# Kernel tuning notes

Measured on AMD Instinct MI355X. Metric: run time of the kernel, lower is better.

## Reference

```python
import jax, jax.numpy as jnp
import numpy as np
from jax import lax

H, HD, P, C, HID = 8, 64, 16, 512, 2048
ALIBI_ALPHA, START_I = 1.0, 0
EPS = 1e-5

def setup_inputs():
    key = jax.random.key(0)
    ks = jax.random.split(key, 20)
    s = 0.02
    return {
        "x": jax.random.normal(ks[0], (8, 1024, C), jnp.float32),
        "Wq": jax.random.normal(ks[1], (HD, HD), jnp.float32) * s,
        "Wk": jax.random.normal(ks[2], (HD, HD), jnp.float32) * s,
        "Wv": jax.random.normal(ks[3], (HD, HD), jnp.float32) * s,
        "Wo": jax.random.normal(ks[4], (C, C), jnp.float32) * s,
        "bo": jnp.zeros((C,), jnp.float32),
        "th_pre": jax.random.normal(ks[5], (H, H), jnp.float32) * (1.0 / np.sqrt(H)),
        "th_post": jax.random.normal(ks[6], (H, H), jnp.float32) * (1.0 / np.sqrt(H)),
        "p_keys": jax.random.normal(ks[7], (P, 1, HD), jnp.float32) * s,
        "p_values": jax.random.normal(ks[8], (P, 1, HD), jnp.float32) * s,
        "conv1_w": jax.random.normal(ks[9], (2 * HID, C, 3), jnp.float32) * s,
        "conv1_b": jnp.zeros((2 * HID,), jnp.float32),
        "conv2_w": jax.random.normal(ks[10], (C, HID, 3), jnp.float32) * s,
        "conv2_b": jnp.zeros((C,), jnp.float32),
        "ln1_g": jnp.ones((C,), jnp.float32),
        "ln1_b": jnp.zeros((C,), jnp.float32),
        "ln2_g": jnp.ones((C,), jnp.float32),
        "ln2_b": jnp.zeros((C,), jnp.float32),
    }

def _layernorm(x, g, b):
    mu = jnp.mean(x, axis=-1, keepdims=True)
    var = jnp.mean((x - mu) ** 2, axis=-1, keepdims=True)
    return (x - mu) * lax.rsqrt(var + EPS) * g + b

def _mha(x, Wq, Wk, Wv, Wo, bo, th_pre, th_post, p_keys, p_values):
    N, L, _ = x.shape
    xh = x.reshape(N, L, H, HD)
    q = xh @ Wq.T  # per-head-dim linear, as in torch (applied to last dim)
    k = xh @ Wk.T
    v = xh @ Wv.T
    # persistent memory: [P,1,HD] broadcast over batch and heads
    pk = jnp.broadcast_to(p_keys[None], (N, P, H, HD))
    pv = jnp.broadcast_to(p_values[None], (N, P, H, HD))
    k = jnp.concatenate([k, pk], axis=1)  # (N, L+P, H, HD)
    v = jnp.concatenate([v, pv], axis=1)
    energy = jnp.einsum('nqhd,nkhd->nhqk', q, k)
    # ALiBi: slope_h = 2^(-alpha*(h+1+start_i)), bias = -|q-k|*slope, zero on persistent cols
    slopes = 2.0 ** (-ALIBI_ALPHA * (jnp.arange(1, H + 1, dtype=jnp.float32) + START_I))
    t = jnp.arange(L, dtype=jnp.float32)
    dist = jnp.abs(t[:, None] - t[None, :])  # (L, L)
    bias = -dist[None, :, :] * slopes[:, None, None]  # (H, L, L)
    bias = jnp.pad(bias, ((0, 0), (0, 0), (0, P)))
    energy = energy + bias[None]
    energy = jnp.einsum('gh,nhqk->ngqk', th_pre, energy)  # pre-softmax talking heads (1x1 conv)
    attn = jax.nn.softmax(energy / jnp.sqrt(jnp.float32(C)), axis=-1)
    attn = jnp.einsum('gh,nhqk->ngqk', th_post, attn)  # post-softmax talking heads
    out = jnp.einsum('nhql,nlhd->nqhd', attn, v).reshape(N, L, C)
    return out @ Wo.T + bo

def _ffn(x, conv1_w, conv1_b, conv2_w, conv2_b):
    dn = ('NCH', 'OIH', 'NCH')
    xc = jnp.transpose(x, (0, 2, 1))  # (N, C, L)
    xp = jnp.pad(xc, ((0, 0), (0, 0), (1, 1)))  # same padding, k=3
    h = lax.conv_general_dilated(xp, conv1_w, (1,), 'VALID', dimension_numbers=dn) + conv1_b[None, :, None]
    h1, h2 = jnp.split(h, 2, axis=1)
    h = jax.nn.silu(h1) * h2  # swiglu
    hp = jnp.pad(h, ((0, 0), (0, 0), (1, 1)))
    y = lax.conv_general_dilated(hp, conv2_w, (1,), 'VALID', dimension_numbers=dn) + conv2_b[None, :, None]
    return jnp.transpose(y, (0, 2, 1))

def reference(x, Wq, Wk, Wv, Wo, bo, th_pre, th_post, p_keys, p_values,
              conv1_w, conv1_b, conv2_w, conv2_b, ln1_g, ln1_b, ln2_g, ln2_b):
    a = _mha(x, Wq, Wk, Wv, Wo, bo, th_pre, th_post, p_keys, p_values)
    x1 = _layernorm(a + x, ln1_g, ln1_b)
    f = _ffn(x1, conv1_w, conv1_b, conv2_w, conv2_b)
    return _layernorm(f + x1, ln2_g, ln2_b)
```

## Files before the change

kernel.cpp:

```cpp
#include <hip/hip_runtime.h>
#include <cstddef>
#include <cstdint>

#define NB   8
#define LQ   1024
#define CH   512
#define HHE  8
#define HDD  64
#define PPM  16
#define LP   1040
#define HID  2048

typedef unsigned short ushort_t;
typedef __attribute__((ext_vector_type(8))) short short8;
typedef __attribute__((ext_vector_type(4))) float floatx4;

static const size_t O_QB   = 0;
static const size_t O_KB   = 2097152;
static const size_t O_VB   = 4227072;
static const size_t O_VT   = 6356992;
static const size_t O_AOB  = 8486912;
static const size_t O_AF   = 10584064;
static const size_t O_X1B  = 16777216;
static const size_t O_HPAD = 18878464;
static const size_t O_W1   = 27283456;
static const size_t O_W2   = 30429184;
static const size_t O_WO   = 32002048;

__device__ __forceinline__ ushort_t f2bf(float f) {
  uint32_t u = __float_as_uint(f);
  u += 0x7FFFu + ((u >> 16) & 1u);
  return (ushort_t)(u >> 16);
}
__device__ __forceinline__ float bf2f(ushort_t h) {
  return __uint_as_float(((uint32_t)h) << 16);
}

__device__ __forceinline__ void async16(ushort_t* lds, const ushort_t* g) {
  __builtin_amdgcn_global_load_lds(
      (const __attribute__((address_space(1))) void*)g,
      (__attribute__((address_space(3))) void*)lds, 16, 0, 0);
}

__global__ __launch_bounds__(256) void pack_bf16_kernel(
    const float* __restrict__ src, ushort_t* __restrict__ dst,
    int K, int KD, int icShift)
{
  const int oc = blockIdx.x;
  const int icMask = (1 << icShift) - 1;
  for (int k = threadIdx.x; k < K; k += 256) {
    int ic = k & icMask, dl = k >> icShift;
    dst[(size_t)oc * K + k] = f2bf(src[(size_t)oc * K + ic * KD + dl]);
  }
}

template<int EPI>
__global__ __launch_bounds__(256, 2) void mfma_gemm(
    const ushort_t* __restrict__ Ab, const ushort_t* __restrict__ Bb,
    int K, int BS, int P, int NOUT,
    const float* __restrict__ bias, const float* __restrict__ res,
    float* __restrict__ outf, ushort_t* __restrict__ outh)
{
  __shared__ ushort_t As[128 * 32];
  __shared__ ushort_t Bs[128 * 32];
  const int t = threadIdx.x;
  const int w = t >> 6, l = t & 63;
  const int m0 = blockIdx.x * 128, n0 = blockIdx.y * 128;

  const int kChunk = K / (int)gridDim.z;
  const int kstart = blockIdx.z * kChunk;

  const int sub = l >> 2;
  const int kc8 = (l & 3) * 8;
  const ushort_t* aptr[2];
  const ushort_t* bptr[2];
  #pragma unroll
  for (int c = 0; c < 2; ++c) {
    int arow = m0 + w * 32 + c * 16 + sub;
    aptr[c] = Ab + (size_t)(arow >> 10) * BS + (size_t)(arow & 1023) * P + kc8 + kstart;
    int brow = n0 + w * 32 + c * 16 + sub;
    bptr[c] = Bb + (size_t)brow * K + kc8 + kstart;
  }

  const int wm = w >> 1, wn = w & 1;
  const int lm = l & 15, q = l >> 4;
  floatx4 acc[4][4];
  #pragma unroll
  for (int i = 0; i < 4; ++i)
    #pragma unroll
    for (int j = 0; j < 4; ++j)
      acc[i][j] = (floatx4){0.f, 0.f, 0.f, 0.f};

  const int kIters = kChunk >> 5;
  for (int kt = 0; kt < kIters; ++kt) {
    __syncthreads();
    async16(&As[w * 1024 +   0], aptr[0]);
    async16(&As[w * 1024 + 512], aptr[1]);
    async16(&Bs[w * 1024 +   0], bptr[0]);
    async16(&Bs[w * 1024 + 512], bptr[1]);
    aptr[0] += 32; aptr[1] += 32; bptr[0] += 32; bptr[1] += 32;
    __syncthreads();
    short8 af[4], bf[4];
    #pragma unroll
    for (int i = 0; i < 4; ++i)
      af[i] = *(const short8*)&As[(wm * 64 + i * 16 + lm) * 32 + q * 8];
    #pragma unroll
    for (int i = 0; i < 4; ++i)
      bf[i] = *(const short8*)&Bs[(wn * 64 + i * 16 + lm) * 32 + q * 8];
    #pragma unroll
    for (int i = 0; i < 4; ++i)
      #pragma unroll
      for (int j = 0; j < 4; ++j)
        acc[i][j] = __builtin_amdgcn_mfma_f32_16x16x32_bf16(af[i], bf[j], acc[i][j], 0, 0, 0);
  }

  #pragma unroll
  for (int i = 0; i < 4; ++i) {
    #pragma unroll
    for (int j = 0; j < 4; ++j) {
      const int mbase = m0 + wm * 64 + i * 16 + q * 4;
      const int n = n0 + wn * 64 + j * 16 + lm;
      #pragma unroll
      for (int r = 0; r < 4; ++r) {
        const int m = mbase + r;
        float v = acc[i][j][r];
        if (EPI == 0) {
          outh[(size_t)m * NOUT + n] = f2bf(v);
        } else if (EPI == 1) {
          outf[(size_t)m * NOUT + n] = v + bias[n];
        } else if (EPI == 2) {
          outf[(size_t)m * NOUT + n] = v + bias[n] + res[(size_t)m * NOUT + n];
        } else {
          outf[(size_t)blockIdx.z * 4194304 + (size_t)m * NOUT + n] = v;
        }
      }
    }
  }
}

__global__ __launch_bounds__(256) void ksum_kernel(
    float* __restrict__ pb, const float* __restrict__ bias)
{
  const size_t i = ((size_t)blockIdx.x * 256 + threadIdx.x) * 4;
  float4 a = *(const float4*)&pb[i];
  float4 b = *(const float4*)&pb[i +  4194304];
  float4 c = *(const float4*)&pb[i +  8388608];
  float4 d = *(const float4*)&pb[i + 12582912];
  const int col = (int)(i & 511);
  float4 bi = *(const float4*)&bias[col];
  float4 o;
  o.x = a.x + b.x + c.x + d.x + bi.x;
  o.y = a.y + b.y + c.y + d.y + bi.y;
  o.z = a.z + b.z + c.z + d.z + bi.z;
  o.w = a.w + b.w + c.w + d.w + bi.w;
  *(float4*)&pb[i] = o;
}

__global__ __launch_bounds__(256) void qkv_mfma(
    const float* __restrict__ x,
    const float* __restrict__ Wq, const float* __restrict__ Wk, const float* __restrict__ Wv,
    ushort_t* __restrict__ qo, ushort_t* __restrict__ ko, ushort_t* __restrict__ vo)
{
  __shared__ ushort_t Ws[8 * 512];
  const int mat = blockIdx.y;
  const float* __restrict__ W = (mat == 0) ? Wq : (mat == 1) ? Wk : Wv;
  const int t = threadIdx.x;

  for (int e = t; e < 4096; e += 256) {
    const int oc = e >> 6, ic = e & 63;
    const int nt = oc >> 4, lmm = oc & 15, s = ic >> 5, qd = (ic >> 3) & 3, j = ic & 7;
    Ws[(((nt * 2 + s) * 4 + qd) * 16 + lmm) * 8 + j] = f2bf(W[e]);
  }

  const int w = t >> 6, l = t & 63;
  const int lm = l & 15, quad = l >> 4;
  const int tok0 = blockIdx.x * 64 + w * 16;

  short8 af[16];
  {
    const float* xrow = x + (size_t)(tok0 + lm) * CH + quad * 8;
    #pragma unroll
    for (int h = 0; h < 8; ++h) {
      #pragma unroll
      for (int s = 0; s < 2; ++s) {
        const float4 a = *(const float4*)(xrow + h * 64 + s * 32);
        const float4 b = *(const float4*)(xrow + h * 64 + s * 32 + 4);
        short8 f;
        f[0] = (short)f2bf(a.x); f[1] = (short)f2bf(a.y);
        f[2] = (short)f2bf(a.z); f[3] = (short)f2bf(a.w);
        f[4] = (short)f2bf(b.x); f[5] = (short)f2bf(b.y);
        f[6] = (short)f2bf(b.z); f[7] = (short)f2bf(b.w);
        af[h * 2 + s] = f;
      }
    }
  }
  __syncthreads();

  short8 bfr[8];
  #pragma unroll
  for (int nt = 0; nt < 4; ++nt)
    #pragma unroll
    for (int s = 0; s < 2; ++s)
      bfr[nt * 2 + s] = *(const short8*)&Ws[((nt * 2 + s) * 64 + l) * 8];

  const int n = tok0 >> 10, lpos = tok0 & 1023;
  ushort_t* outp;
  size_t base;
  if (mat == 0) { base = ((size_t)n * LQ + lpos) * CH; outp = qo; }
  else          { base = ((size_t)n * LP + lpos) * CH; outp = (mat == 1) ? ko : vo; }

  #pragma unroll
  for (int h = 0; h < 8; ++h) {
    floatx4 acc[4];
    #pragma unroll
    for (int nt = 0; nt < 4; ++nt) acc[nt] = (floatx4){0.f, 0.f, 0.f, 0.f};
    #pragma unroll
    for (int nt = 0; nt < 4; ++nt)
      #pragma unroll
      for (int s = 0; s < 2; ++s)
        acc[nt] = __builtin_amdgcn_mfma_f32_16x16x32_bf16(
            af[h * 2 + s], bfr[nt * 2 + s], acc[nt], 0, 0, 0);
    #pragma unroll
    for (int nt = 0; nt < 4; ++nt)
      #pragma unroll
      for (int r = 0; r < 4; ++r)
        outp[base + (size_t)(quad * 4 + r) * CH + h * 64 + nt * 16 + lm] =
            f2bf(acc[nt][r]);
  }
}

__global__ __launch_bounds__(256) void persist_kernel(
    const float* __restrict__ pk, const float* __restrict__ pv,
    ushort_t* __restrict__ ko, ushort_t* __restrict__ vo)
{
  const int t = blockIdx.x * 256 + threadIdx.x;
  const int n = t >> 13, p = (t >> 9) & 15, c = t & 511, d = c & 63;
  const size_t o = ((size_t)n * LP + LQ + p) * CH + c;
  ko[o] = f2bf(pk[p * 64 + d]);
  vo[o] = f2bf(pv[p * 64 + d]);
}

__global__ __launch_bounds__(256) void vtrans_kernel(
    const ushort_t* __restrict__ Vb, ushort_t* __restrict__ VT)
{
  __shared__ ushort_t Ls[16 * 520];
  const int n = blockIdx.y, k0 = blockIdx.x * 16;
  const int t = threadIdx.x;
  const int r = t >> 4;
  {
    const ushort_t* src = Vb + ((size_t)(n * LP + k0 + r)) * 512 + (t & 15) * 8;
    ushort_t* dst = &Ls[r * 520 + (t & 15) * 8];
    #pragma unroll
    for (int it = 0; it < 4; ++it)
      *(short8*)(dst + it * 128) = *(const short8*)(src + it * 128);
  }
  __syncthreads();
  #pragma unroll
  for (int rep = 0; rep < 2; ++rep) {
    const int d = t + rep * 256;
    short8 v0, v1;
    #pragma unroll
    for (int j = 0; j < 8; ++j) {
      v0[j] = (short)Ls[j * 520 + d];
      v1[j] = (short)Ls[(8 + j) * 520 + d];
    }
    ushort_t* dst = VT + ((size_t)(n * 512 + d)) * LP + k0;
    *(short8*)(dst)     = v0;
    *(short8*)(dst + 8) = v1;
  }
}

__global__ __launch_bounds__(256, 2) void attn_mfma(
    const ushort_t* __restrict__ Qb, const ushort_t* __restrict__ Kb,
    const ushort_t* __restrict__ VT,
    const float* __restrict__ thpre, const float* __restrict__ thpost,
    ushort_t* __restrict__ aob)
{
  __shared__ __align__(16) char smem[38912];
  float* Ps  = (float*)smem;
  float* Eb0 = (float*)(smem + 18432);
  float* Eb1 = (float*)(smem + 28672);
  float* Ohn = (float*)smem;

  const int n = blockIdx.y, q0 = blockIdx.x * 16;
  const int t = threadIdx.x;
  const int w = t >> 6, l = t & 63;
  const int lm = l & 15, quad = l >> 4;
  const float invs = 0.044194173824159216f;

  short8 qf[4];
  {
    const ushort_t* qrow = Qb + ((size_t)(n * LQ + q0 + lm)) * 512 + (w * 2) * 64 + quad * 8;
    qf[0] = *(const short8*)(qrow);
    qf[1] = *(const short8*)(qrow + 32);
    qf[2] = *(const short8*)(qrow + 64);
    qf[3] = *(const short8*)(qrow + 96);
  }

  float tps[2][8], psl[2], tpo[2][8];
  #pragma unroll
  for (int gg = 0; gg < 2; ++gg) {
    const int g = w * 2 + gg;
    float ps = 0.f;
    #pragma unroll
    for (int h = 0; h < 8; ++h) {
      float tv = thpre[g * 8 + h] * invs;
      tps[gg][h] = tv;
      ps += tv * (1.0f / (float)(2 << h));
      tpo[gg][h] = thpost[g * 8 + h];
    }
    psl[gg] = ps;
  }

  float m_[2][4], z_[2][4];
  #pragma unroll
  for (int gg = 0; gg < 2; ++gg)
    #pragma unroll
    for (int r = 0; r < 4; ++r) { m_[gg][r] = -1e30f; z_[gg][r] = 0.f; }

  floatx4 o_[2][4];
  #pragma unroll
  for (int gg = 0; gg < 2; ++gg)
    #pragma unroll
    for (int ch = 0; ch < 4; ++ch) o_[gg][ch] = (floatx4){0.f, 0.f, 0.f, 0.f};

  const ushort_t* kg = Kb + ((size_t)(n * LP + lm)) * 512 + (w * 2) * 64 + quad * 8;
  const ushort_t* vg0 = VT + ((size_t)(n * 512) + (w * 2 + 0) * 64 + lm) * LP;
  const ushort_t* vg1 = VT + ((size_t)(n * 512) + (w * 2 + 1) * 64 + lm) * LP;

  short8 kfE[4], kfO[4], vpf[8];

  auto loadKg = [&](short8 (&r)[4], int step) {
    const ushort_t* p = kg + (size_t)step * 8192;
    r[0] = *(const short8*)(p);
    r[1] = *(const short8*)(p + 32);
    r[2] = *(const short8*)(p + 64);
    r[3] = *(const short8*)(p + 96);
  };
  auto loadV = [&](int p) {
    int ko = 32 * p + quad * 8;
    if (ko > 1032) ko = 1032;
    #pragma unroll
    for (int ch = 0; ch < 4; ++ch) {
      vpf[ch]     = *(const short8*)(vg0 + (size_t)(ch * 16) * LP + ko);
      vpf[4 + ch] = *(const short8*)(vg1 + (size_t)(ch * 16) * LP + ko);
    }
  };

  auto qktE = [&](short8 (&kf)[4], float* Eb) {
    #pragma unroll
    for (int hh = 0; hh < 2; ++hh) {
      floatx4 e = (floatx4){0.f, 0.f, 0.f, 0.f};
      e = __builtin_amdgcn_mfma_f32_16x16x32_bf16(qf[hh * 2 + 0], kf[hh * 2 + 0], e, 0, 0, 0);
      e = __builtin_amdgcn_mfma_f32_16x16x32_bf16(qf[hh * 2 + 1], kf[hh * 2 + 1], e, 0, 0, 0);
      *(floatx4*)&Eb[(((w * 2 + hh) * 16 + lm)) * 20 + quad * 4] = e;
    }
  };

  auto online2 = [&](int p) {
    float s0[2][4], s1[2][4];
    #pragma unroll
    for (int gg = 0; gg < 2; ++gg)
      #pragma unroll
      for (int r = 0; r < 4; ++r) { s0[gg][r] = 0.f; s1[gg][r] = 0.f; }
    #pragma unroll
    for (int h = 0; h < 8; ++h) {
      const floatx4 a = *(const floatx4*)&Eb0[(h * 16 + lm) * 20 + quad * 4];
      const floatx4 b = *(const floatx4*)&Eb1[(h * 16 + lm) * 20 + quad * 4];
      #pragma unroll
      for (int gg = 0; gg < 2; ++gg) {
        const float tv = tps[gg][h];
        #pragma unroll
        for (int r = 0; r < 4; ++r) {
          s0[gg][r] += tv * a[r];
          s1[gg][r] += tv * b[r];
        }
      }
    }
    const int k0 = 32 * p;
    float pm[2][4];
    #pragma unroll
    for (int r = 0; r < 4; ++r) {
      const float qpos = (float)(q0 + quad * 4 + r);
      const float d0 = fabsf(qpos - (float)(k0 + lm));
      const float d1 = fabsf(qpos - (float)(k0 + 16 + lm));
      #pragma unroll
      for (int gg = 0; gg < 2; ++gg) {
        s0[gg][r] -= d0 * psl[gg];
        s1[gg][r] -= d1 * psl[gg];
        pm[gg][r] = fmaxf(s0[gg][r], s1[gg][r]);
      }
    }
    #pragma unroll
    for (int off = 1; off < 16; off <<= 1)
      #pragma unroll
      for (int gg = 0; gg < 2; ++gg)
        #pragma unroll
        for (int r = 0; r < 4; ++r)
          pm[gg][r] = fmaxf(pm[gg][r], __shfl_xor(pm[gg][r], off));
    float sc[2][4];
    #pragma unroll
    for (int gg = 0; gg < 2; ++gg)
      #pragma unroll
      for (int r = 0; r < 4; ++r) {
        const float mn = fmaxf(m_[gg][r], pm[gg][r]);
        sc[gg][r] = __expf(m_[gg][r] - mn);
        const float p0 = __expf(s0[gg][r] - mn);
        const float p1 = __expf(s1[gg][r] - mn);
        z_[gg][r] = z_[gg][r] * sc[gg][r] + p0 + p1;
        m_[gg][r] = mn;
        float* prow = &Ps[((w * 2 + gg) * 16 + quad * 4 + r) * 36];
        prow[lm] = p0;
        prow[16 + lm] = p1;
      }
    #pragma unroll
    for (int gg = 0; gg < 2; ++gg)
      #pragma unroll
      for (int ch = 0; ch < 4; ++ch)
        #pragma unroll
        for (int r = 0; r < 4; ++r)
          o_[gg][ch][r] *= sc[gg][r];
  };

  auto online1 = [&]() {
    float s0[2][4];
    #pragma unroll
    for (int gg = 0; gg < 2; ++gg)
      #pragma unroll
      for (int r = 0; r < 4; ++r) s0[gg][r] = 0.f;
    #pragma unroll
    for (int h = 0; h < 8; ++h) {
      const floatx4 a = *(const floatx4*)&Eb0[(h * 16 + lm) * 20 + quad * 4];
      #pragma unroll
      for (int gg = 0; gg < 2; ++gg) {
        const float tv = tps[gg][h];
        #pragma unroll
        for (int r = 0; r < 4; ++r) s0[gg][r] += tv * a[r];
      }
    }
    float pm[2][4];
    #pragma unroll
    for (int gg = 0; gg < 2; ++gg)
      #pragma unroll
      for (int r = 0; r < 4; ++r) pm[gg][r] = s0[gg][r];
    #pragma unroll
    for (int off = 1; off < 16; off <<= 1)
      #pragma unroll
      for (int gg = 0; gg < 2; ++gg)
        #pragma unroll
        for (int r = 0; r < 4; ++r)
          pm[gg][r] = fmaxf(pm[gg][r], __shfl_xor(pm[gg][r], off));
    float sc[2][4];
    #pragma unroll
    for (int gg = 0; gg < 2; ++gg)
      #pragma unroll
      for (int r = 0; r < 4; ++r) {
        const float mn = fmaxf(m_[gg][r], pm[gg][r]);
        sc[gg][r] = __expf(m_[gg][r] - mn);
        const float p0 = __expf(s0[gg][r] - mn);
        z_[gg][r] = z_[gg][r] * sc[gg][r] + p0;
        m_[gg][r] = mn;
        float* prow = &Ps[((w * 2 + gg) * 16 + quad * 4 + r) * 36];
        prow[lm] = p0;
        prow[16 + lm] = 0.f;
      }
    #pragma unroll
    for (int gg = 0; gg < 2; ++gg)
      #pragma unroll
      for (int ch = 0; ch < 4; ++ch)
        #pragma unroll
        for (int r = 0; r < 4; ++r)
          o_[gg][ch][r] *= sc[gg][r];
  };

  auto pv = [&]() {
    #pragma unroll
    for (int gg = 0; gg < 2; ++gg) {
      const float4 pa = *(const float4*)&Ps[((w * 2 + gg) * 16 + lm) * 36 + quad * 8];
      const float4 pb = *(const float4*)&Ps[((w * 2 + gg) * 16 + lm) * 36 + quad * 8 + 4];
      short8 pk;
      pk[0] = (short)f2bf(pa.x); pk[1] = (short)f2bf(pa.y);
      pk[2] = (short)f2bf(pa.z); pk[3] = (short)f2bf(pa.w);
      pk[4] = (short)f2bf(pb.x); pk[5] = (short)f2bf(pb.y);
      pk[6] = (short)f2bf(pb.z); pk[7] = (short)f2bf(pb.w);
      #pragma unroll
      for (int ch = 0; ch < 4; ++ch)
        o_[gg][ch] = __builtin_amdgcn_mfma_f32_16x16x32_bf16(
            pk, vpf[gg * 4 + ch], o_[gg][ch], 0, 0, 0);
    }
  };

  loadKg(kfE, 0);
  loadKg(kfO, 1);
  loadV(0);

  for (int p = 0; p < 32; ++p) {
    qktE(kfE, Eb0);
    qktE(kfO, Eb1);
    loadKg(kfE, 2 * p + 2);
    if (p < 31) loadKg(kfO, 2 * p + 3);
    __syncthreads();
    online2(p);
    __syncthreads();
    pv();
    loadV(p + 1);
  }
  qktE(kfE, Eb0);
  __syncthreads();
  online1();
  __syncthreads();
  pv();

  #pragma unroll
  for (int off = 1; off < 16; off <<= 1)
    #pragma unroll
    for (int gg = 0; gg < 2; ++gg)
      #pragma unroll
      for (int r = 0; r < 4; ++r)
        z_[gg][r] += __shfl_xor(z_[gg][r], off);
  #pragma unroll
  for (int gg = 0; gg < 2; ++gg)
    #pragma unroll
    for (int r = 0; r < 4; ++r) {
      const float zi = 1.0f / z_[gg][r];
      #pragma unroll
      for (int ch = 0; ch < 4; ++ch) o_[gg][ch][r] *= zi;
    }

  __syncthreads();
  #pragma unroll
  for (int gg = 0; gg < 2; ++gg)
    #pragma unroll
    for (int ch = 0; ch < 4; ++ch)
      #pragma unroll
      for (int r = 0; r < 4; ++r)
        Ohn[(w * 2 + gg) * 1088 + (quad * 4 + r) * 68 + ch * 16 + lm] = o_[gg][ch][r];
  __syncthreads();

  float acc[2][4][4];
  #pragma unroll
  for (int gg = 0; gg < 2; ++gg)
    #pragma unroll
    for (int ch = 0; ch < 4; ++ch)
      #pragma unroll
      for (int r = 0; r < 4; ++r) acc[gg][ch][r] = 0.f;
  #pragma unroll
  for (int h = 0; h < 8; ++h) {
    #pragma unroll
    for (int ch = 0; ch < 4; ++ch)
      #pragma unroll
      for (int r = 0; r < 4; ++r) {
        const float ov = Ohn[h * 1088 + (quad * 4 + r) * 68 + ch * 16 + lm];
        acc[0][ch][r] += tpo[0][h] * ov;
        acc[1][ch][r] += tpo[1][h] * ov;
      }
  }

  #pragma unroll
  for (int gg = 0; gg < 2; ++gg)
    #pragma unroll
    for (int ch = 0; ch < 4; ++ch) {
      const int d = (w * 2 + gg) * 64 + ch * 16 + lm;
      #pragma unroll
      for (int r = 0; r < 4; ++r)
        aob[((size_t)(n * LQ + q0 + quad * 4 + r)) * 512 + d] = f2bf(acc[gg][ch][r]);
    }
}

__global__ __launch_bounds__(256) void swiglu_kernel(
    const ushort_t* __restrict__ hraw, const float* __restrict__ bias,
    ushort_t* __restrict__ hpad)
{
  const int tok = blockIdx.x;
  const int n = tok >> 10, l = tok & 1023;
  const int c = threadIdx.x * 8;
  const size_t src = (size_t)tok * 4096 + c;
  const size_t dst = ((size_t)n * 1026 + l + 1) * 2048 + c;
  const short8 h1v = *(const short8*)&hraw[src];
  const short8 h2v = *(const short8*)&hraw[src + 2048];
  const float4 b1a = *(const float4*)&bias[c];
  const float4 b1b = *(const float4*)&bias[c + 4];
  const float4 b2a = *(const float4*)&bias[2048 + c];
  const float4 b2b = *(const float4*)&bias[2048 + c + 4];
  const float bb1[8] = {b1a.x, b1a.y, b1a.z, b1a.w, b1b.x, b1b.y, b1b.z, b1b.w};
  const float bb2[8] = {b2a.x, b2a.y, b2a.z, b2a.w, b2b.x, b2b.y, b2b.z, b2b.w};
  short8 o;
  #pragma unroll
  for (int j = 0; j < 8; ++j) {
    const float h1 = bf2f((ushort_t)h1v[j]) + bb1[j];
    const float h2 = bf2f((ushort_t)h2v[j]) + bb2[j];
    const float s = h1 / (1.f + __expf(-h1));
    o[j] = (short)f2bf(s * h2);
  }
  *(short8*)&hpad[dst] = o;
}

__global__ __launch_bounds__(256) void zero_pads_kernel(
    ushort_t* __restrict__ x1b, ushort_t* __restrict__ hpad)
{
  const int b = blockIdx.x;
  const int n = b >> 1, side = b & 1;
  const size_t r = (size_t)n * 1026 + side * 1025;
  ushort2 z; z.x = 0; z.y = 0;
  *(ushort2*)&x1b[r * 512 + threadIdx.x * 2] = z;
  #pragma unroll
  for (int i = 0; i < 4; ++i)
    *(ushort2*)&hpad[r * 2048 + (threadIdx.x + 256 * i) * 2] = z;
}

__global__ __launch_bounds__(256) void ln_kernel(
    const float* __restrict__ in, const float* __restrict__ res,
    const float* __restrict__ g, const float* __restrict__ b,
    float* __restrict__ outp, ushort_t* __restrict__ bfout)
{
  const int w = threadIdx.x >> 6, lane = threadIdx.x & 63;
  const int tok = blockIdx.x * 4 + w;
  const size_t base = (size_t)tok * CH;
  float4 v0 = *(const float4*)&in[base + (lane << 2)];
  float4 v1 = *(const float4*)&in[base + 256 + (lane << 2)];
  if (res != nullptr) {
    float4 r0 = *(const float4*)&res[base + (lane << 2)];
    float4 r1 = *(const float4*)&res[base + 256 + (lane << 2)];
    v0.x += r0.x; v0.y += r0.y; v0.z += r0.z; v0.w += r0.w;
    v1.x += r1.x; v1.y += r1.y; v1.z += r1.z; v1.w += r1.w;
  }
  float s = v0.x + v0.y + v0.z + v0.w + v1.x + v1.y + v1.z + v1.w;
  #pragma unroll
  for (int off = 32; off > 0; off >>= 1) s += __shfl_xor(s, off);
  const float mu = s * (1.f / 512.f);
  float d0 = v0.x - mu, d1 = v0.y - mu, d2 = v0.z - mu, d3 = v0.w - mu;
  float d4 = v1.x - mu, d5 = v1.y - mu, d6 = v1.z - mu, d7 = v1.w - mu;
  float vs = d0*d0 + d1*d1 + d2*d2 + d3*d3 + d4*d4 + d5*d5 + d6*d6 + d7*d7;
  #pragma unroll
  for (int off = 32; off > 0; off >>= 1) vs += __shfl_xor(vs, off);
  const float r = rsqrtf(vs * (1.f / 512.f) + 1e-5f);
  float4 ga = *(const float4*)&g[(lane << 2)];
  float4 gb = *(const float4*)&g[256 + (lane << 2)];
  float4 ba = *(const float4*)&b[(lane << 2)];
  float4 bb = *(const float4*)&b[256 + (lane << 2)];
  float4 o0, o1;
  o0.x = d0 * r * ga.x + ba.x; o0.y = d1 * r * ga.y + ba.y;
  o0.z = d2 * r * ga.z + ba.z; o0.w = d3 * r * ga.w + ba.w;
  o1.x = d4 * r * gb.x + bb.x; o1.y = d5 * r * gb.y + bb.y;
  o1.z = d6 * r * gb.z + bb.z; o1.w = d7 * r * gb.w + bb.w;
  *(float4*)&outp[base + (lane << 2)] = o0;
  *(float4*)&outp[base + 256 + (lane << 2)] = o1;
  if (bfout != nullptr) {
    const int n = tok >> 10, ll = tok & 1023;
    const size_t bb2 = ((size_t)n * 1026 + ll + 1) * 512;
    ushort4 u0 = make_ushort4(f2bf(o0.x), f2bf(o0.y), f2bf(o0.z), f2bf(o0.w));
    ushort4 u1 = make_ushort4(f2bf(o1.x), f2bf(o1.y), f2bf(o1.z), f2bf(o1.w));
    *(ushort4*)&bfout[bb2 + (lane << 2)] = u0;
    *(ushort4*)&bfout[bb2 + 256 + (lane << 2)] = u1;
  }
}

extern "C" void kernel_launch(void* const* d_in, const int* in_sizes, int n_in,
                              void* d_out, int out_size, void* d_ws, size_t ws_size,
                              hipStream_t stream)
{
  (void)in_sizes; (void)n_in; (void)out_size; (void)ws_size;
  const float* x      = (const float*)d_in[0];
  const float* Wq     = (const float*)d_in[1];
  const float* Wk     = (const float*)d_in[2];
  const float* Wv     = (const float*)d_in[3];
  const float* Wo     = (const float*)d_in[4];
  const float* bo     = (const float*)d_in[5];
  const float* th_pre = (const float*)d_in[6];
  const float* th_post= (const float*)d_in[7];
  const float* p_keys = (const float*)d_in[8];
  const float* p_vals = (const float*)d_in[9];
  const float* c1w    = (const float*)d_in[10];
  const float* c1b    = (const float*)d_in[11];
  const float* c2w    = (const float*)d_in[12];
  const float* c2b    = (const float*)d_in[13];
  const float* ln1g   = (const float*)d_in[14];
  const float* ln1b   = (const float*)d_in[15];
  const float* ln2g   = (const float*)d_in[16];
  const float* ln2b   = (const float*)d_in[17];

  float* ws  = (float*)d_ws;
  float* out = (float*)d_out;

  ushort_t* Qb   = (ushort_t*)(ws + O_QB);
  ushort_t* Kb   = (ushort_t*)(ws + O_KB);
  ushort_t* Vb   = (ushort_t*)(ws + O_VB);
  ushort_t* VT   = (ushort_t*)(ws + O_VT);
  ushort_t* aob  = (ushort_t*)(ws + O_AOB);
  float*    abf  = ws + O_AF;
  ushort_t* x1b  = (ushort_t*)(ws + O_X1B);
  ushort_t* hpad = (ushort_t*)(ws + O_HPAD);
  ushort_t* hraw = (ushort_t*)ws;
  float*    pk4  = ws;
  ushort_t* w1p  = (ushort_t*)(ws + O_W1);
  ushort_t* w2p  = (ushort_t*)(ws + O_W2);
  ushort_t* wop  = (ushort_t*)(ws + O_WO);

  pack_bf16_kernel<<<4096, 256, 0, stream>>>(c1w, w1p, 1536, 3, 9);
  pack_bf16_kernel<<<512,  256, 0, stream>>>(c2w, w2p, 6144, 3, 11);
  pack_bf16_kernel<<<512,  256, 0, stream>>>(Wo,  wop, 512,  1, 9);

  qkv_mfma<<<dim3(128, 3), 256, 0, stream>>>(x, Wq, Wk, Wv, Qb, Kb, Vb);
  persist_kernel<<<256, 256, 0, stream>>>(p_keys, p_vals, Kb, Vb);
  vtrans_kernel<<<dim3(65, 8), 256, 0, stream>>>(Vb, VT);

  attn_mfma<<<dim3(64, 8), 256, 0, stream>>>(Qb, Kb, VT, th_pre, th_post, aob);

  mfma_gemm<2><<<dim3(64, 4), 256, 0, stream>>>(
      aob, wop, 512, 1024 * 512, 512, 512, bo, x, abf, nullptr);

  ln_kernel<<<2048, 256, 0, stream>>>(abf, nullptr, ln1g, ln1b, out, x1b);
  zero_pads_kernel<<<16, 256, 0, stream>>>(x1b, hpad);

  mfma_gemm<0><<<dim3(64, 32), 256, 0, stream>>>(
      x1b, w1p, 1536, 1026 * 512, 512, 4096, nullptr, nullptr, nullptr, hraw);

  swiglu_kernel<<<8192, 256, 0, stream>>>(hraw, c1b, hpad);

  mfma_gemm<3><<<dim3(64, 4, 4), 256, 0, stream>>>(
      hpad, w2p, 6144, 1026 * 2048, 2048, 512, nullptr, nullptr, pk4, nullptr);
  ksum_kernel<<<4096, 256, 0, stream>>>(pk4, c2b);

  ln_kernel<<<2048, 256, 0, stream>>>(pk4, out, ln2g, ln2b, out, nullptr);
}
```

Baseline: 612.4 us.

## Stage V tiles through shared memory with coalesced row loads in attention

```diff
diff --git a/kernel.cpp b/kernel.cpp
--- a/kernel.cpp
+++ b/kernel.cpp
@@ -276,11 +276,12 @@
     const float* __restrict__ thpre, const float* __restrict__ thpost,
     ushort_t* __restrict__ aob)
 {
-  __shared__ __align__(16) char smem[38912];
-  float* Ps  = (float*)smem;
-  float* Eb0 = (float*)(smem + 18432);
-  float* Eb1 = (float*)(smem + 28672);
-  float* Ohn = (float*)smem;
+  __shared__ __align__(16) char smem[79872];
+  ushort_t* Vt  = (ushort_t*)smem;
+  float*    Ps  = (float*)(smem + 40960);
+  float*    Eb0 = (float*)(smem + 59392);
+  float*    Eb1 = (float*)(smem + 69632);
+  float*    Ohn = (float*)smem;
 
   const int n = blockIdx.y, q0 = blockIdx.x * 16;
   const int t = threadIdx.x;
@@ -324,11 +325,11 @@
     #pragma unroll
     for (int ch = 0; ch < 4; ++ch) o_[gg][ch] = (floatx4){0.f, 0.f, 0.f, 0.f};
 
-  const ushort_t* kg = Kb + ((size_t)(n * LP + lm)) * 512 + (w * 2) * 64 + quad * 8;
-  const ushort_t* vg0 = VT + ((size_t)(n * 512) + (w * 2 + 0) * 64 + lm) * LP;
-  const ushort_t* vg1 = VT + ((size_t)(n * 512) + (w * 2 + 1) * 64 + lm) * LP;
-
-  short8 kfE[4], kfO[4], vpf[8];
+  const ushort_t* kg  = Kb + ((size_t)(n * LP + lm)) * 512 + (w * 2) * 64 + quad * 8;
+  const ushort_t* vgA = VT + ((size_t)(n * 512) + t) * LP;
+  const ushort_t* vgB = VT + ((size_t)(n * 512) + t + 256) * LP;
+
+  short8 kfE[4], kfO[4], vX[4], vY[4];
 
   auto loadKg = [&](short8 (&r)[4], int step) {
     const ushort_t* p = kg + (size_t)step * 8192;
@@ -337,14 +338,15 @@
     r[2] = *(const short8*)(p + 64);
     r[3] = *(const short8*)(p + 96);
   };
-  auto loadV = [&](int p) {
-    int ko = 32 * p + quad * 8;
-    if (ko > 1032) ko = 1032;
-    #pragma unroll
-    for (int ch = 0; ch < 4; ++ch) {
-      vpf[ch]     = *(const short8*)(vg0 + (size_t)(ch * 16) * LP + ko);
-      vpf[4 + ch] = *(const short8*)(vg1 + (size_t)(ch * 16) * LP + ko);
-    }
+  auto loadVg = [&](short8 (&r)[4], int off) {
+    r[0] = *(const short8*)(vgA + off); r[1] = *(const short8*)(vgA + off + 8);
+    r[2] = *(const short8*)(vgB + off); r[3] = *(const short8*)(vgB + off + 8);
+  };
+  auto storeV = [&](short8 (&r)[4], int sub) {
+    ushort_t* d0 = &Vt[(size_t)t * 40 + sub * 16];
+    ushort_t* d1 = &Vt[(size_t)(t + 256) * 40 + sub * 16];
+    *(short8*)(d0)     = r[0]; *(short8*)(d0 + 8) = r[1];
+    *(short8*)(d1)     = r[2]; *(short8*)(d1 + 8) = r[3];
   };
 
   auto qktE = [&](short8 (&kf)[4], float* Eb) {
@@ -484,15 +486,18 @@
       pk[4] = (short)f2bf(pb.x); pk[5] = (short)f2bf(pb.y);
       pk[6] = (short)f2bf(pb.z); pk[7] = (short)f2bf(pb.w);
       #pragma unroll
-      for (int ch = 0; ch < 4; ++ch)
-        o_[gg][ch] = __builtin_amdgcn_mfma_f32_16x16x32_bf16(
-            pk, vpf[gg * 4 + ch], o_[gg][ch], 0, 0, 0);
+      for (int ch = 0; ch < 4; ++ch) {
+        const int d = (w * 2 + gg) * 64 + ch * 16 + lm;
+        const short8 vf = *(const short8*)&Vt[d * 40 + quad * 8];
+        o_[gg][ch] = __builtin_amdgcn_mfma_f32_16x16x32_bf16(pk, vf, o_[gg][ch], 0, 0, 0);
+      }
     }
   };
 
   loadKg(kfE, 0);
   loadKg(kfO, 1);
-  loadV(0);
+  loadVg(vX, 0);
+  loadVg(vY, 16);
 
   for (int p = 0; p < 32; ++p) {
     qktE(kfE, Eb0);
@@ -501,13 +506,17 @@
     if (p < 31) loadKg(kfO, 2 * p + 3);
     __syncthreads();
     online2(p);
+    storeV(vX, 0);
+    storeV(vY, 1);
+    loadVg(vX, 32 * (p + 1));
+    if (p < 31) loadVg(vY, 32 * (p + 1) + 16);
     __syncthreads();
     pv();
-    loadV(p + 1);
   }
   qktE(kfE, Eb0);
   __syncthreads();
   online1();
+  storeV(vX, 0);
   __syncthreads();
   pv();
 
```

Result: faster. 530.9 us (-13.3%).
